# Performance work log

Measured on AMD Instinct MI355X. Metric: run time of the kernel, lower is better.

Reference implementation:

```python
import jax, jax.numpy as jnp
import numpy as np

B, S, D, H = 4, 2048, 1024, 16
HD = D // H

def setup_inputs() -> dict:
    key = jax.random.key(0)
    ks = jax.random.split(key, 11)
    s = 1.0 / np.sqrt(D)
    def lin(k):
        kw, kb = jax.random.split(k)
        return (jax.random.uniform(kw, (D, D), jnp.float32, -s, s),
                jax.random.uniform(kb, (D,), jnp.float32, -s, s))
    Wq, bq = lin(ks[0]); Wk, bk = lin(ks[1]); Wv, bv = lin(ks[2]); Wo, bo = lin(ks[3])
    return {
        "query": jax.random.normal(ks[4], (B, S, D), jnp.float32),
        "key": jax.random.normal(ks[5], (B, S, D), jnp.float32),
        "value": jax.random.normal(ks[6], (B, S, D), jnp.float32),
        "Wq": Wq, "bq": bq, "Wk": Wk, "bk": bk,
        "Wv": Wv, "bv": bv, "Wo": Wo, "bo": bo,
    }

def reference(query, key, value, Wq, bq, Wk, bk, Wv, bv, Wo, bo):
    def split_heads(x):  # [B,S,D] -> [B,H,S,HD]
        return x.reshape(B, S, H, HD).transpose(0, 2, 1, 3)
    q = split_heads(query @ Wq + bq)
    k = split_heads(key @ Wk + bk)
    v = split_heads(value @ Wv + bv)
    scores = jnp.einsum('bhqd,bhkd->bhqk', q, k) / np.sqrt(HD)
    probs = jax.nn.softmax(scores, axis=-1)
    ctx = jnp.einsum('bhqk,bhkd->bhqd', probs, v)
    ctx = ctx.transpose(0, 2, 1, 3).reshape(B, S, D)
    return ctx @ Wo + bo
```

## Files before the change

kernel.cpp:

```cpp
#include <hip/hip_runtime.h>
#include <hip/hip_bf16.h>

#define B_ 4
#define S_ 2048
#define D_ 1024
#define H_ 16
#define HD_ 64
#define M_ (B_*S_)

typedef __bf16 bf16;
typedef bf16 bf16x8 __attribute__((ext_vector_type(8)));
typedef bf16 bf16x4 __attribute__((ext_vector_type(4)));
typedef float f32x4 __attribute__((ext_vector_type(4)));

__device__ __forceinline__ void gload_lds16(const void* g, void* l) {
  __builtin_amdgcn_global_load_lds((const __attribute__((address_space(1))) void*)g,
                                   (__attribute__((address_space(3))) void*)l, 16, 0, 0);
}

__global__ __launch_bounds__(256)
void wtrans_kernel(const float* __restrict__ Wq, const float* __restrict__ Wk,
                   const float* __restrict__ Wv, const float* __restrict__ Wo,
                   bf16* __restrict__ Wqt, bf16* __restrict__ Wkt,
                   bf16* __restrict__ Wvt, bf16* __restrict__ Wot) {
  __shared__ float tile[64][65];
  const float* W; bf16* Wt;
  switch (blockIdx.z) {
    case 0: W = Wq; Wt = Wqt; break;
    case 1: W = Wk; Wt = Wkt; break;
    case 2: W = Wv; Wt = Wvt; break;
    default: W = Wo; Wt = Wot; break;
  }
  int n0 = blockIdx.x * 64, k0 = blockIdx.y * 64;
  int tx = threadIdx.x & 63, ty = threadIdx.x >> 6;
#pragma unroll
  for (int i = 0; i < 16; i++) {
    int k = ty + i * 4;
    tile[k][tx] = W[(size_t)(k0 + k) * D_ + n0 + tx];
  }
  __syncthreads();
#pragma unroll
  for (int i = 0; i < 16; i++) {
    int n = ty + i * 4;
    Wt[(size_t)(n0 + n) * D_ + k0 + tx] = (bf16)tile[tx][n];
  }
}

#define QSCALE 0.18033688011112042f

__global__ __launch_bounds__(256)
void proj_gemm_kernel(const float* __restrict__ Aq, const float* __restrict__ Ak,
                      const float* __restrict__ Av,
                      const bf16* __restrict__ Wqt, const bf16* __restrict__ Wkt,
                      const bf16* __restrict__ Wvt,
                      const float* __restrict__ bq, const float* __restrict__ bk,
                      const float* __restrict__ bv,
                      bf16* __restrict__ qb, bf16* __restrict__ kb, bf16* __restrict__ vbT) {
  __shared__ float Asf[128 * 64];
  __shared__ bf16  Bs[128 * 64];
  const float* A; const bf16* Bt; const float* bias;
  if (blockIdx.z == 0)      { A = Aq; Bt = Wqt; bias = bq; }
  else if (blockIdx.z == 1) { A = Ak; Bt = Wkt; bias = bk; }
  else                      { A = Av; Bt = Wvt; bias = bv; }

  const int n0 = blockIdx.x * 128, m0 = blockIdx.y * 128;
  const int tid = threadIdx.x;
  const int lane = tid & 63, w = tid >> 6;
  const int wr = w >> 1, wc = w & 1;
  const int l15 = lane & 15, quad = lane >> 4;
  const int arow_sub = lane >> 4, achk = lane & 15;
  const int brow_sub = lane >> 3, bchk = lane & 7;

  f32x4 acc[4][4] = {};

  for (int kt = 0; kt < D_ / 64; kt++) {
    const int k0 = kt * 64;
#pragma unroll
    for (int t = 0; t < 8; t++) {
      int r0 = w * 32 + t * 4;
      int row = r0 + arow_sub;
      int cg = achk ^ (row & 15);
      gload_lds16(A + (size_t)(m0 + row) * D_ + k0 + cg * 4, &Asf[r0 * 64]);
    }
#pragma unroll
    for (int t = 0; t < 4; t++) {
      int r0 = w * 32 + t * 8;
      int row = r0 + brow_sub;
      int cg = bchk ^ (row & 7);
      gload_lds16(Bt + (size_t)(n0 + row) * D_ + k0 + cg * 8, &Bs[r0 * 64]);
    }
    __syncthreads();

#pragma unroll
    for (int ks = 0; ks < 2; ks++) {
      bf16x8 a[4], b[4];
#pragma unroll
      for (int fm = 0; fm < 4; fm++) {
        int row = wr * 64 + fm * 16 + l15;
        int cl = (ks * 8 + quad * 2) ^ (row & 15);
        f32x4 lo = *(const f32x4*)(&Asf[row * 64 + cl * 4]);
        f32x4 hi = *(const f32x4*)(&Asf[row * 64 + (cl ^ 1) * 4]);
        bf16x8 av;
        av[0] = (bf16)lo[0]; av[1] = (bf16)lo[1]; av[2] = (bf16)lo[2]; av[3] = (bf16)lo[3];
        av[4] = (bf16)hi[0]; av[5] = (bf16)hi[1]; av[6] = (bf16)hi[2]; av[7] = (bf16)hi[3];
        a[fm] = av;
      }
#pragma unroll
      for (int fn = 0; fn < 4; fn++) {
        int row = wc * 64 + fn * 16 + l15;
        b[fn] = *(const bf16x8*)(&Bs[row * 64 + (((ks * 4 + quad) ^ (row & 7)) * 8)]);
      }
#pragma unroll
      for (int fm = 0; fm < 4; fm++)
#pragma unroll
        for (int fn = 0; fn < 4; fn++)
          acc[fm][fn] = __builtin_amdgcn_mfma_f32_16x16x32_bf16(a[fm], b[fn], acc[fm][fn], 0, 0, 0);
    }
    __syncthreads();
  }

  if (blockIdx.z < 2) {
    bf16* C = (blockIdx.z == 0) ? qb : kb;
    float scale = (blockIdx.z == 0) ? QSCALE : 1.0f;
#pragma unroll
    for (int fm = 0; fm < 4; fm++) {
      int row = m0 + wr * 64 + fm * 16 + quad * 4;
#pragma unroll
      for (int fn = 0; fn < 4; fn++) {
        int col = n0 + wc * 64 + fn * 16 + l15;
        float bval = bias[col];
#pragma unroll
        for (int r = 0; r < 4; r++)
          C[(size_t)(row + r) * D_ + col] = (bf16)((acc[fm][fn][r] + bval) * scale);
      }
    }
  } else {
#pragma unroll
    for (int fm = 0; fm < 4; fm++) {
      int row = m0 + wr * 64 + fm * 16 + quad * 4;
#pragma unroll
      for (int fn = 0; fn < 4; fn++) {
        int col = n0 + wc * 64 + fn * 16 + l15;
        float bval = bias[col];
        bf16x4 pk;
#pragma unroll
        for (int r = 0; r < 4; r++) pk[r] = (bf16)(acc[fm][fn][r] + bval);
        *(bf16x4*)(vbT + (size_t)col * M_ + row) = pk;
      }
    }
  }
}

#define LPS 72

__global__ __launch_bounds__(256)
void attn_kernel(const bf16* __restrict__ qb, const bf16* __restrict__ kb,
                 const bf16* __restrict__ vbT, bf16* __restrict__ ctxb) {
  __shared__ bf16 Ks[2][64 * 64];
  __shared__ bf16 Vs[2][64 * 64];
  __shared__ bf16 Ps[128 * LPS];
  __shared__ float Lf[128];

  const int bh = blockIdx.y;
  const int b = bh >> 4, h = bh & 15;
  const int q0 = blockIdx.x * 128;
  const int tid = threadIdx.x, lane = tid & 63, w = tid >> 6;
  const int l15 = lane & 15, quad = lane >> 4;

  const size_t baseQ = ((size_t)(b * S_ + q0)) * D_ + h * HD_;

  bf16x8 qf[2][2];
#pragma unroll
  for (int fm = 0; fm < 2; fm++)
#pragma unroll
    for (int ks = 0; ks < 2; ks++)
      qf[fm][ks] = *(const bf16x8*)(qb + baseQ + (size_t)(w * 32 + fm * 16 + l15) * D_ + ks * 32 + quad * 8);

  f32x4 o[2][4] = {};
  float li[2] = {0.f, 0.f};

  const int srow_i = lane >> 3;
  const int schunk = lane & 7;

  auto stage = [&](int buf, int kt) {
#pragma unroll
    for (int t = 0; t < 2; t++) {
      const int r0 = w * 16 + t * 8;
      const int row = r0 + srow_i;
      const int c = schunk ^ (row & 7);
      const bf16* gK = kb + ((size_t)(b * S_ + kt * 64 + row)) * D_ + h * 64 + c * 8;
      gload_lds16(gK, &Ks[buf][r0 * 64]);
      const bf16* gV = vbT + ((size_t)(h * 64 + row)) * M_ + b * S_ + kt * 64 + c * 8;
      gload_lds16(gV, &Vs[buf][r0 * 64]);
    }
  };

  stage(0, 0);
  __syncthreads();

  for (int kt = 0; kt < S_ / 64; kt++) {
    const int buf = kt & 1;
    if (kt + 1 < S_ / 64) stage(buf ^ 1, kt + 1);

    f32x4 st[4][2] = {};
#pragma unroll
    for (int ks = 0; ks < 2; ks++) {
#pragma unroll
      for (int fk = 0; fk < 4; fk++) {
        const int key = fk * 16 + l15;
        bf16x8 kf = *(const bf16x8*)(&Ks[buf][key * 64 + (((ks * 4 + quad) ^ (key & 7)) * 8)]);
#pragma unroll
        for (int fq = 0; fq < 2; fq++)
          st[fk][fq] = __builtin_amdgcn_mfma_f32_16x16x32_bf16(kf, qf[fq][ks], st[fk][fq], 0, 0, 0);
      }
    }

#pragma unroll
    for (int fq = 0; fq < 2; fq++) {
      const int prow = (w * 32 + fq * 16 + l15) * LPS;
#pragma unroll
      for (int fk = 0; fk < 4; fk++) {
        float p0 = __builtin_amdgcn_exp2f(st[fk][fq][0]);
        float p1 = __builtin_amdgcn_exp2f(st[fk][fq][1]);
        float p2 = __builtin_amdgcn_exp2f(st[fk][fq][2]);
        float p3 = __builtin_amdgcn_exp2f(st[fk][fq][3]);
        li[fq] += (p0 + p1) + (p2 + p3);
        bf16x4 pk;
        pk[0] = (bf16)p0; pk[1] = (bf16)p1; pk[2] = (bf16)p2; pk[3] = (bf16)p3;
        *(bf16x4*)(&Ps[prow + fk * 16 + quad * 4]) = pk;
      }
    }

#pragma unroll
    for (int ks2 = 0; ks2 < 2; ks2++) {
      bf16x8 pf[2], vf[4];
#pragma unroll
      for (int fm = 0; fm < 2; fm++)
        pf[fm] = *(const bf16x8*)(&Ps[(w * 32 + fm * 16 + l15) * LPS + ks2 * 32 + quad * 8]);
#pragma unroll
      for (int fd = 0; fd < 4; fd++) {
        const int d = fd * 16 + l15;
        vf[fd] = *(const bf16x8*)(&Vs[buf][d * 64 + (((ks2 * 4 + quad) ^ (d & 7)) * 8)]);
      }
#pragma unroll
      for (int fm = 0; fm < 2; fm++)
#pragma unroll
        for (int fd = 0; fd < 4; fd++)
          o[fm][fd] = __builtin_amdgcn_mfma_f32_16x16x32_bf16(pf[fm], vf[fd], o[fm][fd], 0, 0, 0);
    }
    __syncthreads();
  }

#pragma unroll
  for (int fq = 0; fq < 2; fq++) {
    float l = li[fq];
    l += __shfl_xor(l, 16);
    l += __shfl_xor(l, 32);
    if (quad == 0) Lf[w * 32 + fq * 16 + l15] = l;
  }
#pragma unroll
  for (int fm = 0; fm < 2; fm++) {
    f32x4 l4 = *(const f32x4*)(&Lf[w * 32 + fm * 16 + quad * 4]);
#pragma unroll
    for (int r = 0; r < 4; r++) {
      float inv = 1.0f / l4[r];
      int row = w * 32 + fm * 16 + quad * 4 + r;
#pragma unroll
      for (int fd = 0; fd < 4; fd++)
        ctxb[baseQ + (size_t)row * D_ + fd * 16 + l15] = (bf16)(o[fm][fd][r] * inv);
    }
  }
}

__global__ __launch_bounds__(256)
void out_gemm_kernel(const bf16* __restrict__ A, const bf16* __restrict__ Bt,
                     const float* __restrict__ bias, float* __restrict__ Cout) {
  __shared__ bf16 As[128 * 64];
  __shared__ bf16 Bs[128 * 64];
  const int n0 = blockIdx.x * 128, m0 = blockIdx.y * 128;
  const int tid = threadIdx.x;
  const int lane = tid & 63, w = tid >> 6;
  const int wr = w >> 1, wc = w & 1;
  const int l15 = lane & 15, quad = lane >> 4;
  const int srow = lane >> 3, schunk = lane & 7;

  f32x4 acc[4][4] = {};

  for (int kt = 0; kt < D_ / 64; kt++) {
    const int k0 = kt * 64;
#pragma unroll
    for (int t = 0; t < 4; t++) {
      int r0 = w * 32 + t * 8;
      int row = r0 + srow;
      int cg = schunk ^ (row & 7);
      gload_lds16(A + (size_t)(m0 + row) * D_ + k0 + cg * 8, &As[r0 * 64]);
      gload_lds16(Bt + (size_t)(n0 + row) * D_ + k0 + cg * 8, &Bs[r0 * 64]);
    }
    __syncthreads();

#pragma unroll
    for (int ks = 0; ks < 2; ks++) {
      bf16x8 a[4], b[4];
#pragma unroll
      for (int fm = 0; fm < 4; fm++) {
        int row = wr * 64 + fm * 16 + l15;
        a[fm] = *(const bf16x8*)(&As[row * 64 + (((ks * 4 + quad) ^ (row & 7)) * 8)]);
      }
#pragma unroll
      for (int fn = 0; fn < 4; fn++) {
        int row = wc * 64 + fn * 16 + l15;
        b[fn] = *(const bf16x8*)(&Bs[row * 64 + (((ks * 4 + quad) ^ (row & 7)) * 8)]);
      }
#pragma unroll
      for (int fm = 0; fm < 4; fm++)
#pragma unroll
        for (int fn = 0; fn < 4; fn++)
          acc[fm][fn] = __builtin_amdgcn_mfma_f32_16x16x32_bf16(a[fm], b[fn], acc[fm][fn], 0, 0, 0);
    }
    __syncthreads();
  }
#pragma unroll
  for (int fm = 0; fm < 4; fm++) {
    int row = m0 + wr * 64 + fm * 16 + quad * 4;
#pragma unroll
    for (int fn = 0; fn < 4; fn++) {
      int col = n0 + wc * 64 + fn * 16 + l15;
      float bval = bias[col];
#pragma unroll
      for (int r = 0; r < 4; r++)
        Cout[(size_t)(row + r) * D_ + col] = acc[fm][fn][r] + bval;
    }
  }
}

extern "C" void kernel_launch(void* const* d_in, const int* in_sizes, int n_in,
                              void* d_out, int out_size, void* d_ws, size_t ws_size,
                              hipStream_t stream) {
  const float* query = (const float*)d_in[0];
  const float* key   = (const float*)d_in[1];
  const float* value = (const float*)d_in[2];
  const float* Wq = (const float*)d_in[3];
  const float* bq = (const float*)d_in[4];
  const float* Wk = (const float*)d_in[5];
  const float* bk = (const float*)d_in[6];
  const float* Wv = (const float*)d_in[7];
  const float* bv = (const float*)d_in[8];
  const float* Wo = (const float*)d_in[9];
  const float* bo = (const float*)d_in[10];
  float* out = (float*)d_out;

  char* ws = (char*)d_ws;
  const size_t WT_BYTES = (size_t)D_ * D_ * sizeof(bf16);
  const size_t MD_BYTES = (size_t)M_ * D_ * sizeof(bf16);
  bf16* Wqt  = (bf16*)(ws);
  bf16* Wkt  = (bf16*)(ws + WT_BYTES);
  bf16* Wvt  = (bf16*)(ws + 2 * WT_BYTES);
  bf16* Wot  = (bf16*)(ws + 3 * WT_BYTES);
  bf16* qb   = (bf16*)(ws + 4 * WT_BYTES);
  bf16* kb   = (bf16*)(ws + 4 * WT_BYTES + MD_BYTES);
  bf16* vbT  = (bf16*)(ws + 4 * WT_BYTES + 2 * MD_BYTES);
  bf16* ctxb = (bf16*)(ws + 4 * WT_BYTES + 3 * MD_BYTES);

  wtrans_kernel<<<dim3(D_ / 64, D_ / 64, 4), 256, 0, stream>>>(
      Wq, Wk, Wv, Wo, Wqt, Wkt, Wvt, Wot);

  proj_gemm_kernel<<<dim3(D_ / 128, M_ / 128, 3), 256, 0, stream>>>(
      query, key, value, Wqt, Wkt, Wvt, bq, bk, bv, qb, kb, vbT);

  attn_kernel<<<dim3(S_ / 128, B_ * H_), 256, 0, stream>>>(qb, kb, vbT, ctxb);

  out_gemm_kernel<<<dim3(D_ / 128, M_ / 128), 256, 0, stream>>>(ctxb, Wot, bo, out);
}
```

Baseline: 379.0 us.

## Enlarge attention query tile, register-prefetch fp32 A in projection, vectorize weight transpose

The attention kernel now handles 256 queries per block with 64 rows per warp, so each staged K/V tile is reused across twice as many queries. It also swizzles the P buffer and replaces the LDS row-sum exchange with shuffles. The projection GEMM now loads fp32 activations into registers one k-step ahead and converts them to bf16 before writing to LDS, which halves LDS footprint and drops the per-fragment conversions. The weight transpose now uses float4 loads and bf16x8 stores. The trade-off is higher register pressure in attention and only 512 attention blocks, which may lower occupancy.

```diff
diff --git a/kernel.cpp b/kernel.cpp
--- a/kernel.cpp
+++ b/kernel.cpp
@@ -23,7 +23,7 @@
                    const float* __restrict__ Wv, const float* __restrict__ Wo,
                    bf16* __restrict__ Wqt, bf16* __restrict__ Wkt,
                    bf16* __restrict__ Wvt, bf16* __restrict__ Wot) {
-  __shared__ float tile[64][65];
+  __shared__ float tile[64][68];
   const float* W; bf16* Wt;
   switch (blockIdx.z) {
     case 0: W = Wq; Wt = Wqt; break;
@@ -31,18 +31,24 @@
     case 2: W = Wv; Wt = Wvt; break;
     default: W = Wo; Wt = Wot; break;
   }
-  int n0 = blockIdx.x * 64, k0 = blockIdx.y * 64;
-  int tx = threadIdx.x & 63, ty = threadIdx.x >> 6;
-#pragma unroll
-  for (int i = 0; i < 16; i++) {
-    int k = ty + i * 4;
-    tile[k][tx] = W[(size_t)(k0 + k) * D_ + n0 + tx];
+  const int n0 = blockIdx.x * 64, k0 = blockIdx.y * 64;
+  const int tid = threadIdx.x;
+#pragma unroll
+  for (int i = 0; i < 4; i++) {
+    int f = tid + i * 256;
+    int k = f >> 4, c = f & 15;
+    float4 v = *(const float4*)(W + (size_t)(k0 + k) * D_ + n0 + c * 4);
+    *(float4*)(&tile[k][c * 4]) = v;
   }
   __syncthreads();
 #pragma unroll
-  for (int i = 0; i < 16; i++) {
-    int n = ty + i * 4;
-    Wt[(size_t)(n0 + n) * D_ + k0 + tx] = (bf16)tile[tx][n];
+  for (int i = 0; i < 2; i++) {
+    int f = tid + i * 256;
+    int n = f >> 3, c = f & 7;
+    bf16x8 o;
+#pragma unroll
+    for (int j = 0; j < 8; j++) o[j] = (bf16)tile[c * 8 + j][n];
+    *(bf16x8*)(Wt + (size_t)(n0 + n) * D_ + k0 + c * 8) = o;
   }
 }
 
@@ -56,8 +62,8 @@
                       const float* __restrict__ bq, const float* __restrict__ bk,
                       const float* __restrict__ bv,
                       bf16* __restrict__ qb, bf16* __restrict__ kb, bf16* __restrict__ vbT) {
-  __shared__ float Asf[128 * 64];
-  __shared__ bf16  Bs[128 * 64];
+  __shared__ bf16 As[128 * 64];
+  __shared__ bf16 Bs[128 * 64];
   const float* A; const bf16* Bt; const float* bias;
   if (blockIdx.z == 0)      { A = Aq; Bt = Wqt; bias = bq; }
   else if (blockIdx.z == 1) { A = Ak; Bt = Wkt; bias = bk; }
@@ -68,28 +74,46 @@
   const int lane = tid & 63, w = tid >> 6;
   const int wr = w >> 1, wc = w & 1;
   const int l15 = lane & 15, quad = lane >> 4;
-  const int arow_sub = lane >> 4, achk = lane & 15;
-  const int brow_sub = lane >> 3, bchk = lane & 7;
+  const int srow = lane >> 3, schunk = lane & 7;
 
   f32x4 acc[4][4] = {};
+  float4 Ar[4][2];
+
+  auto loadA = [&](int kt) {
+    const int k0 = kt * 64;
+#pragma unroll
+    for (int t = 0; t < 4; t++) {
+      const float* p = A + (size_t)(m0 + w * 32 + t * 8 + srow) * D_ + k0 + schunk * 8;
+      Ar[t][0] = *(const float4*)p;
+      Ar[t][1] = *(const float4*)(p + 4);
+    }
+  };
+
+  loadA(0);
 
   for (int kt = 0; kt < D_ / 64; kt++) {
     const int k0 = kt * 64;
 #pragma unroll
-    for (int t = 0; t < 8; t++) {
-      int r0 = w * 32 + t * 4;
-      int row = r0 + arow_sub;
-      int cg = achk ^ (row & 15);
-      gload_lds16(A + (size_t)(m0 + row) * D_ + k0 + cg * 4, &Asf[r0 * 64]);
-    }
-#pragma unroll
     for (int t = 0; t < 4; t++) {
       int r0 = w * 32 + t * 8;
-      int row = r0 + brow_sub;
-      int cg = bchk ^ (row & 7);
+      int row = r0 + srow;
+      int cg = schunk ^ (row & 7);
       gload_lds16(Bt + (size_t)(n0 + row) * D_ + k0 + cg * 8, &Bs[r0 * 64]);
     }
-    __syncthreads();
+#pragma unroll
+    for (int t = 0; t < 4; t++) {
+      int row = w * 32 + t * 8 + srow;
+      int c = schunk ^ (row & 7);
+      bf16x8 v;
+      v[0] = (bf16)Ar[t][0].x; v[1] = (bf16)Ar[t][0].y;
+      v[2] = (bf16)Ar[t][0].z; v[3] = (bf16)Ar[t][0].w;
+      v[4] = (bf16)Ar[t][1].x; v[5] = (bf16)Ar[t][1].y;
+      v[6] = (bf16)Ar[t][1].z; v[7] = (bf16)Ar[t][1].w;
+      *(bf16x8*)(&As[row * 64 + c * 8]) = v;
+    }
+    __syncthreads();
+
+    if (kt + 1 < D_ / 64) loadA(kt + 1);
 
 #pragma unroll
     for (int ks = 0; ks < 2; ks++) {
@@ -97,13 +121,7 @@
 #pragma unroll
       for (int fm = 0; fm < 4; fm++) {
         int row = wr * 64 + fm * 16 + l15;
-        int cl = (ks * 8 + quad * 2) ^ (row & 15);
-        f32x4 lo = *(const f32x4*)(&Asf[row * 64 + cl * 4]);
-        f32x4 hi = *(const f32x4*)(&Asf[row * 64 + (cl ^ 1) * 4]);
-        bf16x8 av;
-        av[0] = (bf16)lo[0]; av[1] = (bf16)lo[1]; av[2] = (bf16)lo[2]; av[3] = (bf16)lo[3];
-        av[4] = (bf16)hi[0]; av[5] = (bf16)hi[1]; av[6] = (bf16)hi[2]; av[7] = (bf16)hi[3];
-        a[fm] = av;
+        a[fm] = *(const bf16x8*)(&As[row * 64 + (((ks * 4 + quad) ^ (row & 7)) * 8)]);
       }
 #pragma unroll
       for (int fn = 0; fn < 4; fn++) {
@@ -150,34 +168,31 @@
     }
   }
 }
-
-#define LPS 72
 
 __global__ __launch_bounds__(256)
 void attn_kernel(const bf16* __restrict__ qb, const bf16* __restrict__ kb,
                  const bf16* __restrict__ vbT, bf16* __restrict__ ctxb) {
   __shared__ bf16 Ks[2][64 * 64];
   __shared__ bf16 Vs[2][64 * 64];
-  __shared__ bf16 Ps[128 * LPS];
-  __shared__ float Lf[128];
+  __shared__ bf16 Ps[256 * 64];
 
   const int bh = blockIdx.y;
   const int b = bh >> 4, h = bh & 15;
-  const int q0 = blockIdx.x * 128;
+  const int q0 = blockIdx.x * 256;
   const int tid = threadIdx.x, lane = tid & 63, w = tid >> 6;
   const int l15 = lane & 15, quad = lane >> 4;
 
   const size_t baseQ = ((size_t)(b * S_ + q0)) * D_ + h * HD_;
 
-  bf16x8 qf[2][2];
-#pragma unroll
-  for (int fm = 0; fm < 2; fm++)
+  bf16x8 qf[4][2];
+#pragma unroll
+  for (int fq = 0; fq < 4; fq++)
 #pragma unroll
     for (int ks = 0; ks < 2; ks++)
-      qf[fm][ks] = *(const bf16x8*)(qb + baseQ + (size_t)(w * 32 + fm * 16 + l15) * D_ + ks * 32 + quad * 8);
-
-  f32x4 o[2][4] = {};
-  float li[2] = {0.f, 0.f};
+      qf[fq][ks] = *(const bf16x8*)(qb + baseQ + (size_t)(w * 64 + fq * 16 + l15) * D_ + ks * 32 + quad * 8);
+
+  f32x4 o[4][4] = {};
+  float li[4] = {};
 
   const int srow_i = lane >> 3;
   const int schunk = lane & 7;
@@ -202,7 +217,7 @@
     const int buf = kt & 1;
     if (kt + 1 < S_ / 64) stage(buf ^ 1, kt + 1);
 
-    f32x4 st[4][2] = {};
+    f32x4 st[4][4] = {};
 #pragma unroll
     for (int ks = 0; ks < 2; ks++) {
 #pragma unroll
@@ -210,14 +225,14 @@
         const int key = fk * 16 + l15;
         bf16x8 kf = *(const bf16x8*)(&Ks[buf][key * 64 + (((ks * 4 + quad) ^ (key & 7)) * 8)]);
 #pragma unroll
-        for (int fq = 0; fq < 2; fq++)
+        for (int fq = 0; fq < 4; fq++)
           st[fk][fq] = __builtin_amdgcn_mfma_f32_16x16x32_bf16(kf, qf[fq][ks], st[fk][fq], 0, 0, 0);
       }
     }
 
 #pragma unroll
-    for (int fq = 0; fq < 2; fq++) {
-      const int prow = (w * 32 + fq * 16 + l15) * LPS;
+    for (int fq = 0; fq < 4; fq++) {
+      const int row = w * 64 + fq * 16 + l15;
 #pragma unroll
       for (int fk = 0; fk < 4; fk++) {
         float p0 = __builtin_amdgcn_exp2f(st[fk][fq][0]);
@@ -227,23 +242,26 @@
         li[fq] += (p0 + p1) + (p2 + p3);
         bf16x4 pk;
         pk[0] = (bf16)p0; pk[1] = (bf16)p1; pk[2] = (bf16)p2; pk[3] = (bf16)p3;
-        *(bf16x4*)(&Ps[prow + fk * 16 + quad * 4]) = pk;
+        const int chunk = (fk * 2 + (quad >> 1)) ^ (row & 7);
+        *(bf16x4*)(&Ps[row * 64 + chunk * 8 + (quad & 1) * 4]) = pk;
       }
     }
 
 #pragma unroll
     for (int ks2 = 0; ks2 < 2; ks2++) {
-      bf16x8 pf[2], vf[4];
-#pragma unroll
-      for (int fm = 0; fm < 2; fm++)
-        pf[fm] = *(const bf16x8*)(&Ps[(w * 32 + fm * 16 + l15) * LPS + ks2 * 32 + quad * 8]);
+      bf16x8 pf[4], vf[4];
+#pragma unroll
+      for (int fm = 0; fm < 4; fm++) {
+        const int row = w * 64 + fm * 16 + l15;
+        pf[fm] = *(const bf16x8*)(&Ps[row * 64 + (((ks2 * 4 + quad) ^ (row & 7)) * 8)]);
+      }
 #pragma unroll
       for (int fd = 0; fd < 4; fd++) {
         const int d = fd * 16 + l15;
         vf[fd] = *(const bf16x8*)(&Vs[buf][d * 64 + (((ks2 * 4 + quad) ^ (d & 7)) * 8)]);
       }
 #pragma unroll
-      for (int fm = 0; fm < 2; fm++)
+      for (int fm = 0; fm < 4; fm++)
 #pragma unroll
         for (int fd = 0; fd < 4; fd++)
           o[fm][fd] = __builtin_amdgcn_mfma_f32_16x16x32_bf16(pf[fm], vf[fd], o[fm][fd], 0, 0, 0);
@@ -251,23 +269,23 @@
     __syncthreads();
   }
 
-#pragma unroll
-  for (int fq = 0; fq < 2; fq++) {
+  float linv[4];
+#pragma unroll
+  for (int fq = 0; fq < 4; fq++) {
     float l = li[fq];
     l += __shfl_xor(l, 16);
     l += __shfl_xor(l, 32);
-    if (quad == 0) Lf[w * 32 + fq * 16 + l15] = l;
-  }
-#pragma unroll
-  for (int fm = 0; fm < 2; fm++) {
-    f32x4 l4 = *(const f32x4*)(&Lf[w * 32 + fm * 16 + quad * 4]);
+    linv[fq] = 1.0f / l;
+  }
+#pragma unroll
+  for (int fq = 0; fq < 4; fq++) {
 #pragma unroll
     for (int r = 0; r < 4; r++) {
-      float inv = 1.0f / l4[r];
-      int row = w * 32 + fm * 16 + quad * 4 + r;
+      float inv = __shfl(linv[fq], quad * 4 + r);
+      int row = w * 64 + fq * 16 + quad * 4 + r;
 #pragma unroll
       for (int fd = 0; fd < 4; fd++)
-        ctxb[baseQ + (size_t)row * D_ + fd * 16 + l15] = (bf16)(o[fm][fd][r] * inv);
+        ctxb[baseQ + (size_t)row * D_ + fd * 16 + l15] = (bf16)(o[fq][fd][r] * inv);
     }
   }
 }
@@ -367,7 +385,7 @@
   proj_gemm_kernel<<<dim3(D_ / 128, M_ / 128, 3), 256, 0, stream>>>(
       query, key, value, Wqt, Wkt, Wvt, bq, bk, bv, qb, kb, vbT);
 
-  attn_kernel<<<dim3(S_ / 128, B_ * H_), 256, 0, stream>>>(qb, kb, vbT, ctxb);
+  attn_kernel<<<dim3(S_ / 256, B_ * H_), 256, 0, stream>>>(qb, kb, vbT, ctxb);
 
   out_gemm_kernel<<<dim3(D_ / 128, M_ / 128), 256, 0, stream>>>(ctxb, Wot, bo, out);
 }
```

Result: slower. 388.9 us (+2.6%).
